# Optimization experiments

Measured on AMD Instinct MI355X. Metric: run time of the kernel, lower is better.

Reference implementation:

```python
import jax, jax.numpy as jnp
import numpy as np
from jax import lax

N_SIN = 3

def _bn(x, g, b, m, v, eps):
    sh = [1] * x.ndim; sh[1] = -1
    r = lambda t: t.reshape(sh)
    return (x - r(m)) / jnp.sqrt(r(v) + eps) * r(g) + r(b)

def _conv2d(x, w, b, padding):
    y = lax.conv_general_dilated(x, w, (1, 1), padding,
                                 dimension_numbers=('NCHW', 'OIHW', 'NCHW'))
    return y + b[None, :, None, None]

def _causal_conv1d(x, w, b):
    k = w.shape[-1]
    y = lax.conv_general_dilated(x, w, (1,), [(k - 1, 0)],
                                 dimension_numbers=('NCH', 'OIH', 'NCH'))
    return y + b[None, :, None]

def _se(x, w1, w2):
    y = x.mean(axis=2)                                   # [B,C] global avg pool
    y = jax.nn.sigmoid(jax.nn.relu(y @ w1.T) @ w2.T)
    return x * y[:, :, None]

def _kan(x, W1, W2, B1, B2):
    # x: [B,din]; per-edge tiny MLP: sin/cos embed -> linear -> silu -> linear
    omega = (2.0 ** jnp.arange(N_SIN)).astype(x.dtype)   # [n_sin]
    ox = x[..., None] * omega                            # [B,din,n_sin]
    feat = jnp.concatenate([x[..., None], jnp.sin(ox), jnp.cos(ox)], axis=-1)  # [B,din,7]
    h = jnp.einsum('bif,ijhf->bijh', feat, W1) + B1[None]  # [B,din,dout,h]
    h = jax.nn.silu(h)
    out = jnp.einsum('bijh,ijh->bij', h, W2[:, :, 0, :]) + B2[None, :, :, 0]
    return out.sum(axis=1)                               # [B,dout]

def _lstm(x, w_ih, w_hh, b_ih, b_hh):
    B, T, E = x.shape
    H = w_hh.shape[1]
    def step(carry, xt):
        h, c = carry
        g = xt @ w_ih.T + h @ w_hh.T + (b_ih + b_hh)
        i, f, gg, o = jnp.split(g, 4, axis=-1)           # torch gate order i,f,g,o
        c = jax.nn.sigmoid(f) * c + jax.nn.sigmoid(i) * jnp.tanh(gg)
        h = jax.nn.sigmoid(o) * jnp.tanh(c)
        return (h, c), h
    init = (jnp.zeros((B, H), x.dtype), jnp.zeros((B, H), x.dtype))
    _, hs = lax.scan(step, init, jnp.swapaxes(x, 0, 1))
    return jnp.swapaxes(hs, 0, 1)                        # [B,T,H]

def _cluster(hidden):
    B, T, H = hidden.shape
    last = hidden[:, -1, :]
    hn = hidden / jnp.maximum(jnp.linalg.norm(hidden, axis=-1, keepdims=True), 1e-8)
    sim = jnp.einsum('bth,bsh->bts', hn, hn)
    sim = jnp.exp(-5.5 * (1.0 - sim))
    sim = sim * (1.0 - jnp.eye(T, dtype=sim.dtype))      # zero diagonal
    # 2-D prefix sums replace the O(T) python loop over block means
    S = jnp.cumsum(jnp.cumsum(sim, axis=1), axis=2)
    Sii = jnp.diagonal(S, axis1=1, axis2=2)[:, :T - 1]   # sum of [:i,:i]
    R = S[:, -1, :T - 1]                                 # sum of [:, :i]
    C = S[:, :T - 1, -1]                                 # sum of [:i, :]
    tot = S[:, -1, -1][:, None]
    i_f = jnp.arange(1, T, dtype=sim.dtype)
    dist = (Sii / i_f**2
            + (tot - R - C + Sii) / (T - i_f)**2
            - (C - Sii) / (i_f * (T - i_f))
            - (R - Sii) / (i_f * (T - i_f)))             # [B,T-1]
    cuts = jnp.argmax(dist, axis=1) + 1                  # [B]
    mask = (jnp.arange(T)[None, :] < cuts[:, None]).astype(hidden.dtype)
    corr = (hidden * mask[:, :, None]).sum(axis=1) / cuts[:, None].astype(hidden.dtype)
    return last, corr

def reference(x, we1, be1, bn_e1_g, bn_e1_b, bn_e1_m, bn_e1_v, we2, be2, bn_e2_g, bn_e2_b, bn_e2_m, bn_e2_v, w_ih, w_hh, b_ih, b_hh, mu_W1, mu_W2, mu_B1, mu_B2, std_W1, std_W2, std_B1, std_B2, muc_W1, muc_W2, muc_B1, muc_B2, stdc_W1, stdc_W2, stdc_B1, stdc_B2, fc_W1, fc_W2, fc_B1, fc_B2, wc1, bc1, bn1_g, bn1_b, bn1_m, bn1_v, se1_w1, se1_w2, wc2, bc2, bn2_g, bn2_b, bn2_m, bn2_v, se2_w1, se2_w2, wc3, bc3, bn3_g, bn3_b, bn3_m, bn3_v, eps1, eps2):
    gelu = lambda t: jax.nn.gelu(t, approximate=False)
    x = jnp.transpose(x, (0, 2, 1))                      # shuffle: [B,T,F]->[B,F,T]
    h2d = _conv2d(x[:, None], we1, be1, 'SAME')          # [B,4E,F,T]
    h2d = gelu(_bn(h2d, bn_e1_g, bn_e1_b, bn_e1_m, bn_e1_v, 1e-5))
    h2d = _conv2d(h2d, we2, be2, 'VALID')                # [B,E,1,T]
    h2d = gelu(_bn(h2d, bn_e2_g, bn_e2_b, bn_e2_m, bn_e2_v, 1e-5))
    x_src = jnp.transpose(h2d[:, :, 0, :], (0, 2, 1))    # [B,T,E]
    hseq = _lstm(x_src, w_ih, w_hh, b_ih, b_hh)          # [B,T,H]
    out, corr = _cluster(hseq)
    mu = _kan(corr, mu_W1, mu_W2, mu_B1, mu_B2)
    std = jax.nn.softplus(_kan(corr, std_W1, std_W2, std_B1, std_B2) - 5.0)
    z = mu + std * eps1
    x_z = jnp.concatenate([out, z], axis=1)              # [B,2H]
    mu_c = _kan(x_z, muc_W1, muc_W2, muc_B1, muc_B2)
    std_c = jax.nn.softplus(_kan(x_z, stdc_W1, stdc_W2, stdc_B1, stdc_B2) - 5.0)
    x1 = mu_c + std_c * eps2                             # dropout = identity (eval)
    x2 = jnp.transpose(x, (0, 2, 1))                     # [B,T,F]: channels = seq_len
    x2 = gelu(_bn(_causal_conv1d(x2, wc1, bc1), bn1_g, bn1_b, bn1_m, bn1_v, 1e-3))
    x2 = _se(x2, se1_w1, se1_w2)
    x2 = gelu(_bn(_causal_conv1d(x2, wc2, bc2), bn2_g, bn2_b, bn2_m, bn2_v, 1e-3))
    x2 = _se(x2, se2_w1, se2_w2)
    x2 = gelu(_bn(_causal_conv1d(x2, wc3, bc3), bn3_g, bn3_b, bn3_m, bn3_v, 1e-3))
    x2 = x2.mean(axis=2)                                 # [B,conv3_nf]
    x_all = jnp.concatenate([x1, x2], axis=1)            # [B, H+conv3_nf]
    return _kan(x_all, fc_W1, fc_W2, fc_B1, fc_B2)       # [B,num_classes]

def setup_inputs():
    key = jax.random.key(0)
    ks = iter(jax.random.split(key, 128))
    f32 = jnp.float32
    def n(shape, s=0.05):
        return s * jax.random.normal(next(ks), shape, f32)
    def bn_params(c):
        g = 1.0 + 0.05 * jax.random.normal(next(ks), (c,), f32)
        b = 0.05 * jax.random.normal(next(ks), (c,), f32)
        m = 0.05 * jax.random.normal(next(ks), (c,), f32)
        v = jax.random.uniform(next(ks), (c,), f32, 0.5, 1.5)
        return g, b, m, v
    def kan_params(din, dout, h=32, feat=1 + 2 * N_SIN):
        s = (2.0 / (feat + h)) ** 0.5
        return (n((din, dout, h, feat), s), n((din, dout, 1, h), s),
                jnp.zeros((din, dout, h), f32), jnp.zeros((din, dout, 1), f32))
    B, T, F_, E, H = 32, 256, 32, 64, 128
    inp = {}
    inp['x'] = jax.random.normal(next(ks), (B, T, F_), f32)
    inp['we1'] = n((4 * E, 1, 1, 8)); inp['be1'] = n((4 * E,))
    inp['bn_e1_g'], inp['bn_e1_b'], inp['bn_e1_m'], inp['bn_e1_v'] = bn_params(4 * E)
    inp['we2'] = n((E, 4 * E, F_, 1)); inp['be2'] = n((E,))
    inp['bn_e2_g'], inp['bn_e2_b'], inp['bn_e2_m'], inp['bn_e2_v'] = bn_params(E)
    inp['w_ih'] = n((4 * H, E)); inp['w_hh'] = n((4 * H, H))
    inp['b_ih'] = n((4 * H,)); inp['b_hh'] = n((4 * H,))
    for nm, (di, do) in [('mu', (H, H)), ('std', (H, H)), ('muc', (2 * H, H)), ('stdc', (2 * H, H)), ('fc', (2 * H, 10))]:
        w1, w2, b1, b2 = kan_params(di, do)
        inp[nm + '_W1'], inp[nm + '_W2'], inp[nm + '_B1'], inp[nm + '_B2'] = w1, w2, b1, b2
    inp['wc1'] = n((128, T, 8)); inp['bc1'] = n((128,))
    inp['bn1_g'], inp['bn1_b'], inp['bn1_m'], inp['bn1_v'] = bn_params(128)
    inp['se1_w1'] = n((8, 128)); inp['se1_w2'] = n((128, 8))
    inp['wc2'] = n((256, 128, 5)); inp['bc2'] = n((256,))
    inp['bn2_g'], inp['bn2_b'], inp['bn2_m'], inp['bn2_v'] = bn_params(256)
    inp['se2_w1'] = n((16, 256)); inp['se2_w2'] = n((256, 16))
    inp['wc3'] = n((128, 256, 3)); inp['bc3'] = n((128,))
    inp['bn3_g'], inp['bn3_b'], inp['bn3_m'], inp['bn3_v'] = bn_params(128)
    inp['eps1'] = jax.random.normal(next(ks), (B, H), f32)
    inp['eps2'] = jax.random.normal(next(ks), (B, H), f32)
    return inp
```

## Files before the change

### kernel.cpp

```cpp
#include <hip/hip_runtime.h>
#include <hip/hip_bf16.h>
#include <math.h>

typedef __hip_bfloat16 bf16;

#define DEV static __device__ __forceinline__

DEV float geluf(float x){ return 0.5f*x*(1.0f + erff(x*0.70710678118654752f)); }
DEV float sigmf(float x){ return 1.0f/(1.0f + __expf(-x)); }
DEV float softplusf(float x){ return (x > 15.f) ? x : log1pf(__expf(x)); }
DEV float tanhfast(float x){ float e = __expf(2.f*x); return fmaf(-2.f, 1.f/(e+1.f), 1.f); }

typedef __attribute__((ext_vector_type(8))) short v8s;
typedef __attribute__((ext_vector_type(4))) float v4f;
typedef _Float16 f16;
typedef f16 h2 __attribute__((ext_vector_type(2)));
typedef f16 f16x8 __attribute__((ext_vector_type(8)));
typedef unsigned u32x4 __attribute__((ext_vector_type(4)));

DEV float dot2f(h2 a, h2 b, float c){
#if __has_builtin(__builtin_amdgcn_fdot2)
  return __builtin_amdgcn_fdot2(a, b, c, false);
#else
  return fmaf((float)a.y, (float)b.y, fmaf((float)a.x, (float)b.x, c));
#endif
}

DEV h2 geth2(f16x8 v, int j){ h2 r; r.x = v[2*j]; r.y = v[2*j+1]; return r; }

DEV void lds_barrier(){
  asm volatile("s_waitcnt lgkmcnt(0)" ::: "memory");
  __builtin_amdgcn_s_barrier();
  __builtin_amdgcn_sched_barrier(0);
}

enum : size_t {
  OFF_W1F   = 0,
  OFF_B1F   = 2048,
  OFF_S2E   = 2304,
  OFF_B2E   = 2368,
  OFF_WIHT  = 2432,
  OFF_BIASG = 35200,
  OFF_WHHT  = 35712,
  OFF_EPI1S = 101248,
  OFF_EPI1B = 101376,
  OFF_EPI2S = 101504,
  OFF_EPI2B = 101760,
  OFF_EPI3S = 102016,
  OFF_EPI3B = 102144,
  OFF_WE2B  = 102272,
  OFF_XSRC  = 364416,
  OFF_GX    = 888704,
  OFF_HSEQ  = 5083008,
  OFF_HN    = 6131584,
  OFF_PCOL  = 7180160,
  OFF_CCOL  = 7188352,
  OFF_CUTS  = 7196544,
  OFF_LAST  = 7196576,
  OFF_CORR  = 7200672,
  OFF_FEATA = 7204768,
  OFF_MUO   = 7233440,
  OFF_STDO  = 7237536,
  OFF_XZ    = 7241632,
  OFF_FEATB = 7249824,
  OFF_MUCO  = 7307168,
  OFF_STDCO = 7311264,
  OFF_XC1   = 7315360,
  OFF_XC2   = 7446432,
  OFF_KP    = 7708576,
  OFF_B2S   = 7741344,
  OFF_X2F   = 7839648,
  OFF_XALL  = 7843744,
  OFF_FEATC = 7851936,
  WS_FLOATS = 7909280
};

__global__ __launch_bounds__(256) void prep_kernel(
    const float* we1, const float* be1,
    const float* e1g, const float* e1b, const float* e1m, const float* e1v,
    const float* we2, const float* be2, const float* e2g, const float* e2b, const float* e2m, const float* e2v,
    const float* wih, const float* whh, const float* bih, const float* bhh,
    const float* bc1, const float* c1g, const float* c1b, const float* c1m, const float* c1v,
    const float* bc2, const float* c2g, const float* c2b, const float* c2m, const float* c2v,
    const float* bc3, const float* c3g, const float* c3b, const float* c3m, const float* c3v,
    const float* muB2, const float* sdB2, const float* mcB2, const float* scB2, const float* fcB2,
    float* ws)
{
  int idx = blockIdx.x*256 + threadIdx.x;
  if(idx < 2048){
    int o = idx>>3;
    float s = e1g[o] * rsqrtf(e1v[o] + 1e-5f);
    ws[OFF_W1F + idx] = we1[idx] * s;
  } else if(idx < 2304){
    int o = idx - 2048;
    float s = e1g[o] * rsqrtf(e1v[o] + 1e-5f);
    ws[OFF_B1F + o] = s*(be1[o] - e1m[o]) + e1b[o];
  } else if(idx < 2368){
    int e = idx - 2304;
    float s = e2g[e] * rsqrtf(e2v[e] + 1e-5f);
    ws[OFF_S2E + e] = s;
    ws[OFF_B2E + e] = s*(be2[e] - e2m[e]) + e2b[e];
  } else if(idx < 35136){
    int q = idx - 2368; int e = q>>9, g = q&511;
    ws[OFF_WIHT + q] = wih[g*64 + e];
  } else if(idx < 35648){
    int g = idx - 35136;
    ws[OFF_BIASG + g] = bih[g] + bhh[g];
  } else if(idx < 101184){
    int q = idx - 35648;
    if(q < 32768){
      int k2 = q>>9, g = q&511;
      h2 v;
      v.x = (f16)whh[g*128 + 2*k2];
      v.y = (f16)whh[g*128 + 2*k2 + 1];
      ((h2*)(ws + OFF_WHHT))[g*64 + k2] = v;
    }
  } else if(idx < 101312){
    int o = idx - 101184;
    float s = c1g[o] * rsqrtf(c1v[o] + 1e-3f);
    ws[OFF_EPI1S + o] = s;
    ws[OFF_EPI1B + o] = s*(bc1[o] - c1m[o]) + c1b[o];
  } else if(idx < 101568){
    int o = idx - 101312;
    float s = c2g[o] * rsqrtf(c2v[o] + 1e-3f);
    ws[OFF_EPI2S + o] = s;
    ws[OFF_EPI2B + o] = s*(bc2[o] - c2m[o]) + c2b[o];
  } else if(idx < 101696){
    int o = idx - 101568;
    float s = c3g[o] * rsqrtf(c3v[o] + 1e-3f);
    ws[OFF_EPI3S + o] = s;
    ws[OFF_EPI3B + o] = s*(bc3[o] - c3m[o]) + c3b[o];
  } else if(idx < 625984){
    int q = idx - 101696;
    int o = q >> 11, rem = q & 2047;
    int e = rem >> 5, f = rem & 31;
    bf16* Wr = (bf16*)(ws + OFF_WE2B);
    Wr[q] = __float2bfloat16(we2[(size_t)e*8192 + o*32 + f]);
  } else if(idx < 626112){
    int j = idx - 625984; float s = 0.f;
    for(int i=0;i<128;i++) s += muB2[i*128+j];
    ws[OFF_B2S + j] = s;
  } else if(idx < 626240){
    int j = idx - 626112; float s = 0.f;
    for(int i=0;i<128;i++) s += sdB2[i*128+j];
    ws[OFF_B2S + 128 + j] = s;
  } else if(idx < 626368){
    int j = idx - 626240; float s = 0.f;
    for(int i=0;i<256;i++) s += mcB2[i*128+j];
    ws[OFF_B2S + 256 + j] = s;
  } else if(idx < 626496){
    int j = idx - 626368; float s = 0.f;
    for(int i=0;i<256;i++) s += scB2[i*128+j];
    ws[OFF_B2S + 384 + j] = s;
  } else if(idx < 626506){
    int j = idx - 626496; float s = 0.f;
    for(int i=0;i<256;i++) s += fcB2[i*10+j];
    ws[OFF_B2S + 512 + j] = s;
  }
}

__global__ __launch_bounds__(256,1) void encoder_kernel(
    const float* __restrict__ x, const float* __restrict__ w1f, const float* __restrict__ b1f,
    const float* __restrict__ s2e, const float* __restrict__ b2e,
    const bf16* __restrict__ Wr, float* __restrict__ x_src)
{
  __shared__ float xs[39*32];
  __shared__ float w1s[2048];
  __shared__ float b1s[256];
  __shared__ __align__(16) unsigned short At[2][32*136];
  __shared__ __align__(16) unsigned short Bt[2][4*2560];

  int blk = blockIdx.x; int b = blk>>3; int t0 = (blk&7)*32;
  int tid = threadIdx.x;

  for(int i=tid;i<2048;i+=256) w1s[i] = w1f[i];
  b1s[tid] = b1f[tid];
  for(int i=tid;i<39*32;i+=256){
    int r=i>>5, f=i&31; int t=t0-3+r;
    xs[i] = (t>=0 && t<256) ? x[(b*256+t)*32+f] : 0.f;
  }
  __syncthreads();

  int f = tid & 31, tq = tid >> 5;
  int lane = tid & 63, w = tid >> 6;
  int wm = w & 1, wn = w >> 1;
  int m0 = wm*16, n0 = wn*32;
  int l15 = lane & 15, quad = lane >> 4;

  const v8s* Wv = (const v8s*)Wr;

  auto stage = [&](int cc, int buf){
    v8s bw[4];
    #pragma unroll
    for(int i=0;i<4;i++) bw[i] = Wv[cc*1024 + i*256 + tid];
    unsigned short aval[16];
    #pragma unroll
    for(int ol=0;ol<4;ol++){
      int o = cc*4 + ol;
      float wv[8];
      #pragma unroll
      for(int j=0;j<8;j++) wv[j] = w1s[o*8+j];
      float bb = b1s[o];
      #pragma unroll
      for(int i=0;i<4;i++){
        int tl = tq*4 + i;
        float c = bb;
        #pragma unroll
        for(int j=0;j<8;j++) c = fmaf(wv[j], xs[(tl+j)*32+f], c);
        aval[ol*4+i] = ((__hip_bfloat16_raw)__float2bfloat16(geluf(c))).x;
      }
    }
    #pragma unroll
    for(int ol=0;ol<4;ol++){
      #pragma unroll
      for(int i=0;i<4;i++)
        At[buf][(tq*4+i)*136 + ol*32 + f] = aval[ol*4+i];
    }
    #pragma unroll
    for(int i=0;i<4;i++){
      int j = i*256 + tid;
      int ol = j>>8, e = (j&255)>>2, f8 = j&3;
      *(v8s*)&Bt[buf][ol*2560 + e*40 + f8*8] = bw[i];
    }
  };

  stage(0, 0);
  __syncthreads();

  v4f acc0 = {0.f,0.f,0.f,0.f}, acc1 = {0.f,0.f,0.f,0.f};

  for(int c=0;c<64;c++){
    int p = c & 1, q = p ^ 1;
    if(c < 63) stage(c+1, q);
    #pragma unroll
    for(int ol=0;ol<4;ol++){
      v8s av = *(const v8s*)&At[p][(m0+l15)*136 + ol*32 + quad*8];
      v8s b0 = *(const v8s*)&Bt[p][ol*2560 + (n0+l15)*40 + quad*8];
      v8s b1 = *(const v8s*)&Bt[p][ol*2560 + (n0+16+l15)*40 + quad*8];
      acc0 = __builtin_amdgcn_mfma_f32_16x16x32_bf16(av, b0, acc0, 0, 0, 0);
      acc1 = __builtin_amdgcn_mfma_f32_16x16x32_bf16(av, b1, acc1, 0, 0, 0);
    }
    __syncthreads();
  }

  #pragma unroll
  for(int r=0;r<4;r++){
    int t = t0 + m0 + quad*4 + r;
    int e0 = n0 + l15;
    float v0 = geluf(s2e[e0]*acc0[r] + b2e[e0]);
    x_src[((size_t)(b*256+t))*64 + e0] = v0;
    int e1 = e0 + 16;
    float v1 = geluf(s2e[e1]*acc1[r] + b2e[e1]);
    x_src[((size_t)(b*256+t))*64 + e1] = v1;
  }
}

__global__ __launch_bounds__(256) void gates_kernel(
    const float* x_src, const float* wihT, const float* biasg, float* gx)
{
  __shared__ float xsh[32*64];
  int blk = blockIdx.x; int b = blk>>3, t0 = (blk&7)*32;
  int tid = threadIdx.x;
  for(int i=tid;i<2048;i+=256) xsh[i] = x_src[((size_t)b*256+t0)*64 + i];
  __syncthreads();
  int g0 = tid, g1 = tid + 256;
  float acc0[32], acc1[32];
  #pragma unroll
  for(int tt=0;tt<32;tt++){ acc0[tt]=0.f; acc1[tt]=0.f; }
  for(int e=0;e<64;e++){
    float w0 = wihT[e*512+g0], w1 = wihT[e*512+g1];
    #pragma unroll
    for(int tt=0;tt<32;tt++){
      float xv = xsh[tt*64+e];
      acc0[tt] = fmaf(xv, w0, acc0[tt]);
      acc1[tt] = fmaf(xv, w1, acc1[tt]);
    }
  }
  float bg0 = biasg[g0], bg1 = biasg[g1];
  #pragma unroll
  for(int tt=0;tt<32;tt++){
    gx[((size_t)b*256+t0+tt)*512 + g0] = acc0[tt] + bg0;
    gx[((size_t)b*256+t0+tt)*512 + g1] = acc1[tt] + bg1;
  }
}

#define LSTM_STEP(GI, GF, GG, GO, PR, PW, T)                                 \
  {                                                                          \
    const f16x8* hp = (const f16x8*)&hsh[PR][half*64];                       \
    f16x8 hvv[8];                                                            \
    _Pragma("unroll")                                                        \
    for(int q=0;q<8;q++) hvv[q] = hp[q];                                     \
    float si=0.f, sf=0.f, sg=0.f, so=0.f;                                    \
    _Pragma("unroll")                                                        \
    for(int q=0;q<8;q++){                                                    \
      f16x8 Wi = __builtin_bit_cast(f16x8, wi[q]);                           \
      f16x8 Wf = __builtin_bit_cast(f16x8, wf[q]);                           \
      f16x8 Wg = __builtin_bit_cast(f16x8, wg[q]);                           \
      f16x8 Wo = __builtin_bit_cast(f16x8, wo[q]);                           \
      f16x8 hq = hvv[q];                                                     \
      _Pragma("unroll")                                                      \
      for(int j=0;j<4;j++){                                                  \
        h2 hj = geth2(hq, j);                                                \
        si = dot2f(hj, geth2(Wi,j), si);                                     \
        sf = dot2f(hj, geth2(Wf,j), sf);                                     \
        sg = dot2f(hj, geth2(Wg,j), sg);                                     \
        so = dot2f(hj, geth2(Wo,j), so);                                     \
      }                                                                      \
    }                                                                        \
    si += __shfl_xor(si, 32, 64);                                            \
    sf += __shfl_xor(sf, 32, 64);                                            \
    sg += __shfl_xor(sg, 32, 64);                                            \
    so += __shfl_xor(so, 32, 64);                                            \
    float iv = sigmf(si + (GI));                                             \
    float fv = sigmf(sf + (GF));                                             \
    float gv = tanhfast(sg + (GG));                                          \
    float ov = sigmf(so + (GO));                                             \
    c = fmaf(fv, c, iv*gv);                                                  \
    float h = ov*tanhfast(c);                                                \
    if(half == 0){                                                           \
      hsh[PW][n] = (f16)h;                                                   \
      hseq[((size_t)b*256+(T))*128 + n] = h;                                 \
    }                                                                        \
    lds_barrier();                                                           \
  }

__global__ __launch_bounds__(256)
__attribute__((amdgpu_waves_per_eu(1,1)))
void lstm_conv_kernel(
    const float* __restrict__ gates_x, const float* __restrict__ whh16f, float* __restrict__ hseq,
    const float* __restrict__ x,
    const float* __restrict__ wc1, const float* __restrict__ wc2, const float* __restrict__ wc3,
    const float* __restrict__ epi1s, const float* __restrict__ epi1b,
    const float* __restrict__ epi2s, const float* __restrict__ epi2b,
    const float* __restrict__ epi3s, const float* __restrict__ epi3b,
    const float* __restrict__ se1w1, const float* __restrict__ se1w2,
    const float* __restrict__ se2w1, const float* __restrict__ se2w2,
    float* __restrict__ x2f)
{
  __shared__ __align__(16) f16 hsh[2][128];
  __shared__ float bufA[8192];
  __shared__ float bufB[4096];
  __shared__ float msh[256];
  __shared__ float ysh[16];

  int tid = threadIdx.x;
  if(blockIdx.x < 32){
    int b = blockIdx.x;
    int wave = tid >> 6, lane = tid & 63;
    int half = lane >> 5;
    int n = wave*32 + (lane & 31);

    const u32x4* Wp = (const u32x4*)whh16f;
    u32x4 wi[8], wf[8], wg[8], wo[8];
    #pragma unroll
    for(int q=0;q<8;q++){
      wi[q] = Wp[(size_t)(n      )*16 + half*8 + q];
      wf[q] = Wp[(size_t)(n + 128)*16 + half*8 + q];
      wg[q] = Wp[(size_t)(n + 256)*16 + half*8 + q];
      wo[q] = Wp[(size_t)(n + 384)*16 + half*8 + q];
    }
    asm volatile("" :
      "+v"(wi[0]), "+v"(wi[1]), "+v"(wi[2]), "+v"(wi[3]),
      "+v"(wi[4]), "+v"(wi[5]), "+v"(wi[6]), "+v"(wi[7]),
      "+v"(wf[0]), "+v"(wf[1]), "+v"(wf[2]), "+v"(wf[3]),
      "+v"(wf[4]), "+v"(wf[5]), "+v"(wf[6]), "+v"(wf[7]));
    asm volatile("" :
      "+v"(wg[0]), "+v"(wg[1]), "+v"(wg[2]), "+v"(wg[3]),
      "+v"(wg[4]), "+v"(wg[5]), "+v"(wg[6]), "+v"(wg[7]),
      "+v"(wo[0]), "+v"(wo[1]), "+v"(wo[2]), "+v"(wo[3]),
      "+v"(wo[4]), "+v"(wo[5]), "+v"(wo[6]), "+v"(wo[7]));

    if(tid < 128) hsh[0][tid] = (f16)0.f;
    float c = 0.f;
    const float* gx = gates_x + (size_t)b*256*512;
    float i0v = gx[n], f0v = gx[128+n], g0v = gx[256+n], o0v = gx[384+n];
    float i1v = gx[512+n], f1v = gx[512+128+n], g1v = gx[512+256+n], o1v = gx[512+384+n];
    __syncthreads();
    for(int t=0; t<256; t+=2){
      float i2v=0.f,f2v=0.f,g2v=0.f,o2v=0.f,i3v=0.f,f3v=0.f,g3v=0.f,o3v=0.f;
      if(t+2 < 256){
        const float* gp = gx + (size_t)(t+2)*512;
        i2v = gp[n]; f2v = gp[128+n]; g2v = gp[256+n]; o2v = gp[384+n];
      }
      LSTM_STEP(i0v, f0v, g0v, o0v, 0, 1, t);
      if(t+3 < 256){
        const float* gp = gx + (size_t)(t+3)*512;
        i3v = gp[n]; f3v = gp[128+n]; g3v = gp[256+n]; o3v = gp[384+n];
      }
      LSTM_STEP(i1v, f1v, g1v, o1v, 1, 0, t+1);
      i0v=i2v; f0v=f2v; g0v=g2v; o0v=o2v;
      i1v=i3v; f1v=f3v; g1v=g3v; o1v=o3v;
    }
  } else {
    int cb = blockIdx.x - 32;
    for(int i=tid; i<8192; i+=256) bufA[i] = x[(size_t)cb*8192 + i];
    __syncthreads();

    {
      int o = tid >> 1, lh = tid & 1, l0 = lh*16;
      float acc[16];
      #pragma unroll
      for(int j=0;j<16;j++) acc[j]=0.f;
      const float* wrow = wc1 + (size_t)o*2048;
      for(int c=0;c<256;c++){
        float wv[8];
        #pragma unroll
        for(int k=0;k<8;k++) wv[k] = wrow[c*8+k];
        float xr[23];
        #pragma unroll
        for(int i=0;i<23;i++){
          int li = l0 - 7 + i;
          xr[i] = (li>=0) ? bufA[c*32+li] : 0.f;
        }
        #pragma unroll
        for(int j=0;j<16;j++){
          #pragma unroll
          for(int k=0;k<8;k++) acc[j] = fmaf(xr[j+k], wv[k], acc[j]);
        }
      }
      float s = epi1s[o], bb = epi1b[o];
      float g[16]; float m = 0.f;
      #pragma unroll
      for(int j=0;j<16;j++){ g[j] = geluf(s*acc[j]+bb); m += g[j]; }
      m += __shfl_xor(m, 1, 64);
      if(lh==0) msh[o] = m*(1.f/32.f);
      __syncthreads();
      if(tid < 8){
        float t2=0.f;
        for(int k=0;k<128;k++) t2 = fmaf(msh[k], se1w1[tid*128+k], t2);
        ysh[tid] = fmaxf(t2, 0.f);
      }
      __syncthreads();
      float t2=0.f;
      #pragma unroll
      for(int k=0;k<8;k++) t2 = fmaf(ysh[k], se1w2[o*8+k], t2);
      float sc = sigmf(t2);
      #pragma unroll
      for(int j=0;j<16;j++) bufB[o*32 + l0 + j] = g[j]*sc;
      __syncthreads();
    }

    {
      int o = tid;
      float acc[32];
      #pragma unroll
      for(int j=0;j<32;j++) acc[j]=0.f;
      const float* wrow = wc2 + (size_t)o*640;
      for(int c=0;c<128;c++){
        float wv[5];
        #pragma unroll
        for(int k=0;k<5;k++) wv[k] = wrow[c*5+k];
        float xr[36];
        #pragma unroll
        for(int i=0;i<36;i++){
          int li = i - 4;
          xr[i] = (li>=0) ? bufB[c*32+li] : 0.f;
        }
        #pragma unroll
        for(int j=0;j<32;j++){
          #pragma unroll
          for(int k=0;k<5;k++) acc[j] = fmaf(xr[j+k], wv[k], acc[j]);
        }
      }
      float s = epi2s[o], bb = epi2b[o];
      float m = 0.f;
      #pragma unroll
      for(int j=0;j<32;j++){ acc[j] = geluf(s*acc[j]+bb); m += acc[j]; }
      msh[o] = m*(1.f/32.f);
      __syncthreads();
      if(tid < 16){
        float t2=0.f;
        for(int k=0;k<256;k++) t2 = fmaf(msh[k], se2w1[tid*256+k], t2);
        ysh[tid] = fmaxf(t2, 0.f);
      }
      __syncthreads();
      float t2=0.f;
      #pragma unroll
      for(int k=0;k<16;k++) t2 = fmaf(ysh[k], se2w2[o*16+k], t2);
      float sc = sigmf(t2);
      #pragma unroll
      for(int j=0;j<32;j++) bufA[o*32 + j] = acc[j]*sc;
      __syncthreads();
    }

    {
      int o = tid >> 1, lh = tid & 1, l0 = lh*16;
      float acc[16];
      #pragma unroll
      for(int j=0;j<16;j++) acc[j]=0.f;
      const float* wrow = wc3 + (size_t)o*768;
      for(int c=0;c<256;c++){
        float wv[3];
        #pragma unroll
        for(int k=0;k<3;k++) wv[k] = wrow[c*3+k];
        float xr[18];
        #pragma unroll
        for(int i=0;i<18;i++){
          int li = l0 - 2 + i;
          xr[i] = (li>=0) ? bufA[c*32+li] : 0.f;
        }
        #pragma unroll
        for(int j=0;j<16;j++){
          #pragma unroll
          for(int k=0;k<3;k++) acc[j] = fmaf(xr[j+k], wv[k], acc[j]);
        }
      }
      float s = epi3s[o], bb = epi3b[o];
      float m = 0.f;
      #pragma unroll
      for(int j=0;j<16;j++) m += geluf(s*acc[j]+bb);
      m += __shfl_xor(m, 1, 64);
      if(lh==0) x2f[cb*128 + o] = m*(1.f/32.f);
    }
  }
}

__global__ __launch_bounds__(64) void hn_kernel(const float* hseq, float* hn)
{
  size_t row = blockIdx.x; int lane = threadIdx.x;
  const float* hp = hseq + row*128;
  float v0 = hp[lane], v1 = hp[lane+64];
  float ss = v0*v0 + v1*v1;
  #pragma unroll
  for(int m=1;m<64;m<<=1) ss += __shfl_xor(ss, m, 64);
  float r = 1.f / fmaxf(sqrtf(ss), 1e-8f);
  hn[row*128 + lane]      = v0*r;
  hn[row*128 + 64 + lane] = v1*r;
}

__global__ __launch_bounds__(256) void pc_kernel(const float* hn, float* pcol, float* ccol)
{
  int blk = blockIdx.x; int b = blk>>3, chunk = blk&7;
  int tid = threadIdx.x; int il = tid & 31, ts = tid >> 5;
  int i = chunk*32 + il;
  const float4* hb = (const float4*)(hn + (size_t)b*32768);
  float4 hi[32];
  #pragma unroll
  for(int r=0;r<32;r++) hi[r] = hb[(size_t)i*32 + r];
  float ps=0.f, cs=0.f;
  for(int t=ts*32; t<ts*32+32; t++){
    float dx=0.f, dy=0.f, dz=0.f, dw=0.f;
    #pragma unroll
    for(int r=0;r<32;r++){
      float4 hv = hb[(size_t)t*32 + r];
      dx = fmaf(hi[r].x, hv.x, dx);
      dy = fmaf(hi[r].y, hv.y, dy);
      dz = fmaf(hi[r].z, hv.z, dz);
      dw = fmaf(hi[r].w, hv.w, dw);
    }
    float dot = (dx+dy)+(dz+dw);
    float sim = (t==i) ? 0.f : expf(-5.5f*(1.0f - dot));
    cs += sim;
    if(t < i) ps += sim;
  }
  __shared__ float red[16][32];
  red[ts][il] = ps; red[8+ts][il] = cs;
  __syncthreads();
  if(tid < 32){
    float s=0.f;
    for(int r=0;r<8;r++) s += red[r][tid];
    pcol[b*256 + chunk*32 + tid] = s;
  } else if(tid < 64){
    int c2 = tid - 32; float s=0.f;
    for(int r=0;r<8;r++) s += red[8+r][c2];
    ccol[b*256 + chunk*32 + c2] = s;
  }
}

__global__ __launch_bounds__(256) void cutcorr_kernel(
    const float* pcol, const float* ccol, const float* hseq,
    float* last, float* corr, int* cuts)
{
  int b = blockIdx.x, tid = threadIdx.x;
  __shared__ float D[256], RC[256], dist[256];
  __shared__ int cutsh;
  if(tid == 0){
    float d=0.f, r=0.f;
    for(int i=0;i<256;i++){
      d += 2.f*pcol[b*256+i]; D[i]=d;
      r += ccol[b*256+i];     RC[i]=r;
    }
  }
  __syncthreads();
  float tot = RC[255];
  if(tid < 255){
    float Dv = D[tid], Rv = RC[tid];
    float i_f = (float)(tid+1), j_f = 256.f - i_f;
    dist[tid] = Dv/(i_f*i_f) + (tot - 2.f*Rv + Dv)/(j_f*j_f) - 2.f*(Rv - Dv)/(i_f*j_f);
  }
  __syncthreads();
  if(tid == 0){
    float best = dist[0]; int bi = 0;
    for(int i=1;i<255;i++) if(dist[i] > best){ best = dist[i]; bi = i; }
    cutsh = bi + 1; cuts[b] = cutsh;
  }
  __syncthreads();
  int cut = cutsh;
  int k = tid & 127, half = tid >> 7;
  float s = 0.f;
  for(int t=half; t<cut; t+=2) s += hseq[((size_t)b*256+t)*128 + k];
  __shared__ float partial[2][128];
  partial[half][k] = s;
  __syncthreads();
  if(tid < 128){
    corr[b*128+tid] = (partial[0][tid] + partial[1][tid]) / (float)cut;
    last[b*128+tid] = hseq[((size_t)b*256+255)*128 + tid];
  }
}

__global__ __launch_bounds__(256) void feat_kernel(const float* xin, float* feat, int n)
{
  int idx = blockIdx.x*256 + threadIdx.x;
  if(idx >= n) return;
  float xv = xin[idx];
  float* fp = feat + (size_t)idx*7;
  fp[0]=xv;
  fp[1]=sinf(xv); fp[2]=sinf(2.f*xv); fp[3]=sinf(4.f*xv);
  fp[4]=cosf(xv); fp[5]=cosf(2.f*xv); fp[6]=cosf(4.f*xv);
}

__global__ __launch_bounds__(256) void kanp2_kernel(
    const float* __restrict__ feat,
    const float* __restrict__ W1a, const float* __restrict__ B1a, const float* __restrict__ W2a,
    const float* __restrict__ W1b, const float* __restrict__ B1b, const float* __restrict__ W2b,
    int din, int dout, float* __restrict__ partial, int pstride)
{
  __shared__ float feat_s[32*225];
  __shared__ float red[8][32];
  int z = blockIdx.z;
  const float* W1 = z ? W1b : W1a;
  const float* B1 = z ? B1b : B1a;
  const float* W2 = z ? W2b : W2a;
  partial += (size_t)z * pstride;
  int j = blockIdx.x, ic = blockIdx.y;
  int i0 = ic*32;
  int tid = threadIdx.x;
  int b = tid & 31, hg = tid >> 5;
  for(int q=tid; q<1792; q+=256){
    int br = q/56, qq = q - br*56;
    float4 v = *(const float4*)(feat + ((size_t)br*din + i0)*7 + qq*4);
    float* d = &feat_s[br*225 + qq*4];
    d[0]=v.x; d[1]=v.y; d[2]=v.z; d[3]=v.w;
  }
  __syncthreads();
  float acc = 0.f;
  const float* fb = &feat_s[b*225];
  for(int ii=0; ii<32; ii++){
    int i = i0 + ii;
    size_t hbase = ((size_t)i*dout + j)*32 + hg*4;
    const float4* w1p = (const float4*)(W1 + ((size_t)i*dout + j)*224 + hg*28);
    float w1a[28];
    #pragma unroll
    for(int q=0;q<7;q++) *(float4*)&w1a[q*4] = w1p[q];
    float4 b1v = *(const float4*)(B1 + hbase);
    float4 w2v = *(const float4*)(W2 + hbase);
    float f[7];
    #pragma unroll
    for(int q=0;q<7;q++) f[q] = fb[ii*7+q];
    float b1a[4] = {b1v.x, b1v.y, b1v.z, b1v.w};
    float w2a[4] = {w2v.x, w2v.y, w2v.z, w2v.w};
    #pragma unroll
    for(int hh=0;hh<4;hh++){
      float hv = b1a[hh];
      #pragma unroll
      for(int q=0;q<7;q++) hv = fmaf(f[q], w1a[hh*7+q], hv);
      float sv = hv / (1.f + __expf(-hv));
      acc = fmaf(sv, w2a[hh], acc);
    }
  }
  red[hg][b] = acc;
  __syncthreads();
  if(tid < 32){
    float s = 0.f;
    #pragma unroll
    for(int q=0;q<8;q++) s += red[q][tid];
    partial[((size_t)ic*32 + tid)*dout + j] = s;
  }
}

__global__ __launch_bounds__(256) void kanp_kernel(
    const float* __restrict__ feat, const float* __restrict__ W1,
    const float* __restrict__ B1, const float* __restrict__ W2,
    int din, int dout, float* __restrict__ partial)
{
  __shared__ float feat_s[32*225];
  __shared__ float red[8][32];
  int j = blockIdx.x, ic = blockIdx.y;
  int i0 = ic*32;
  int tid = threadIdx.x;
  int b = tid & 31, hg = tid >> 5;
  for(int q=tid; q<1792; q+=256){
    int br = q/56, qq = q - br*56;
    float4 v = *(const float4*)(feat + ((size_t)br*din + i0)*7 + qq*4);
    float* d = &feat_s[br*225 + qq*4];
    d[0]=v.x; d[1]=v.y; d[2]=v.z; d[3]=v.w;
  }
  __syncthreads();
  float acc = 0.f;
  const float* fb = &feat_s[b*225];
  for(int ii=0; ii<32; ii++){
    int i = i0 + ii;
    size_t hbase = ((size_t)i*dout + j)*32 + hg*4;
    const float4* w1p = (const float4*)(W1 + ((size_t)i*dout + j)*224 + hg*28);
    float w1a[28];
    #pragma unroll
    for(int q=0;q<7;q++) *(float4*)&w1a[q*4] = w1p[q];
    float4 b1v = *(const float4*)(B1 + hbase);
    float4 w2v = *(const float4*)(W2 + hbase);
    float f[7];
    #pragma unroll
    for(int q=0;q<7;q++) f[q] = fb[ii*7+q];
    float b1a[4] = {b1v.x, b1v.y, b1v.z, b1v.w};
    float w2a[4] = {w2v.x, w2v.y, w2v.z, w2v.w};
    #pragma unroll
    for(int hh=0;hh<4;hh++){
      float hv = b1a[hh];
      #pragma unroll
      for(int q=0;q<7;q++) hv = fmaf(f[q], w1a[hh*7+q], hv);
      float sv = hv / (1.f + __expf(-hv));
      acc = fmaf(sv, w2a[hh], acc);
    }
  }
  red[hg][b] = acc;
  __syncthreads();
  if(tid < 32){
    float s = 0.f;
    #pragma unroll
    for(int q=0;q<8;q++) s += red[q][tid];
    partial[((size_t)ic*32 + tid)*dout + j] = s;
  }
}

__global__ __launch_bounds__(256) void kanr_kernel(
    const float* __restrict__ partial, const float* __restrict__ b2s,
    int NI, int dout, float* __restrict__ outp)
{
  int idx = blockIdx.x*256 + threadIdx.x;
  if(idx >= 32*dout) return;
  int b = idx / dout, j = idx - b*dout;
  float s = b2s[j];
  for(int ic=0; ic<NI; ic++) s += partial[((size_t)ic*32 + b)*dout + j];
  outp[idx] = s;
}

__global__ __launch_bounds__(256) void kanrz_kernel(
    const float* __restrict__ kp, const float* __restrict__ b2s,
    const float* __restrict__ eps1, const float* __restrict__ last, float* __restrict__ xz)
{
  int idx = blockIdx.x*256 + threadIdx.x;
  if(idx >= 4096) return;
  int b = idx >> 7, j = idx & 127;
  float mu = b2s[j], sd = b2s[128+j];
  #pragma unroll
  for(int ic=0; ic<4; ic++){
    mu += kp[((size_t)ic*32 + b)*128 + j];
    sd += kp[16384 + ((size_t)ic*32 + b)*128 + j];
  }
  float z = mu + softplusf(sd - 5.f)*eps1[idx];
  xz[b*256 + j]       = last[idx];
  xz[b*256 + 128 + j] = z;
}

__global__ __launch_bounds__(256) void kanrx_kernel(
    const float* __restrict__ kp, const float* __restrict__ b2s,
    const float* __restrict__ eps2, const float* __restrict__ x2f, float* __restrict__ xa)
{
  int idx = blockIdx.x*256 + threadIdx.x;
  if(idx >= 4096) return;
  int b = idx >> 7, j = idx & 127;
  float mu = b2s[256+j], sd = b2s[384+j];
  #pragma unroll
  for(int ic=0; ic<8; ic++){
    mu += kp[((size_t)ic*32 + b)*128 + j];
    sd += kp[32768 + ((size_t)ic*32 + b)*128 + j];
  }
  xa[b*256 + j]       = mu + softplusf(sd - 5.f)*eps2[idx];
  xa[b*256 + 128 + j] = x2f[idx];
}

extern "C" void kernel_launch(void* const* d_in, const int* in_sizes, int n_in,
                              void* d_out, int out_size, void* d_ws, size_t ws_size,
                              hipStream_t stream)
{
  const float* x    = (const float*)d_in[0];
  const float* we1  = (const float*)d_in[1];
  const float* be1  = (const float*)d_in[2];
  const float* e1g  = (const float*)d_in[3];
  const float* e1b  = (const float*)d_in[4];
  const float* e1m  = (const float*)d_in[5];
  const float* e1v  = (const float*)d_in[6];
  const float* we2  = (const float*)d_in[7];
  const float* be2  = (const float*)d_in[8];
  const float* e2g  = (const float*)d_in[9];
  const float* e2b  = (const float*)d_in[10];
  const float* e2m  = (const float*)d_in[11];
  const float* e2v  = (const float*)d_in[12];
  const float* wih  = (const float*)d_in[13];
  const float* whh  = (const float*)d_in[14];
  const float* bih  = (const float*)d_in[15];
  const float* bhh  = (const float*)d_in[16];
  const float* muW1 = (const float*)d_in[17];
  const float* muW2 = (const float*)d_in[18];
  const float* muB1 = (const float*)d_in[19];
  const float* muB2 = (const float*)d_in[20];
  const float* sdW1 = (const float*)d_in[21];
  const float* sdW2 = (const float*)d_in[22];
  const float* sdB1 = (const float*)d_in[23];
  const float* sdB2 = (const float*)d_in[24];
  const float* mcW1 = (const float*)d_in[25];
  const float* mcW2 = (const float*)d_in[26];
  const float* mcB1 = (const float*)d_in[27];
  const float* mcB2 = (const float*)d_in[28];
  const float* scW1 = (const float*)d_in[29];
  const float* scW2 = (const float*)d_in[30];
  const float* scB1 = (const float*)d_in[31];
  const float* scB2 = (const float*)d_in[32];
  const float* fcW1 = (const float*)d_in[33];
  const float* fcW2 = (const float*)d_in[34];
  const float* fcB1 = (const float*)d_in[35];
  const float* fcB2 = (const float*)d_in[36];
  const float* wc1  = (const float*)d_in[37];
  const float* bc1  = (const float*)d_in[38];
  const float* c1g  = (const float*)d_in[39];
  const float* c1b  = (const float*)d_in[40];
  const float* c1m  = (const float*)d_in[41];
  const float* c1v  = (const float*)d_in[42];
  const float* se1w1= (const float*)d_in[43];
  const float* se1w2= (const float*)d_in[44];
  const float* wc2  = (const float*)d_in[45];
  const float* bc2  = (const float*)d_in[46];
  const float* c2g  = (const float*)d_in[47];
  const float* c2b  = (const float*)d_in[48];
  const float* c2m  = (const float*)d_in[49];
  const float* c2v  = (const float*)d_in[50];
  const float* se2w1= (const float*)d_in[51];
  const float* se2w2= (const float*)d_in[52];
  const float* wc3  = (const float*)d_in[53];
  const float* bc3  = (const float*)d_in[54];
  const float* c3g  = (const float*)d_in[55];
  const float* c3b  = (const float*)d_in[56];
  const float* c3m  = (const float*)d_in[57];
  const float* c3v  = (const float*)d_in[58];
  const float* eps1 = (const float*)d_in[59];
  const float* eps2 = (const float*)d_in[60];

  float* ws = (float*)d_ws;
  float* kp   = ws + OFF_KP;
  float* kp2  = ws + OFF_GX;
  float* b2s  = ws + OFF_B2S;

  prep_kernel<<<2448, 256, 0, stream>>>(we1, be1, e1g,e1b,e1m,e1v,
      we2, be2,e2g,e2b,e2m,e2v, wih,whh,bih,bhh,
      bc1,c1g,c1b,c1m,c1v, bc2,c2g,c2b,c2m,c2v, bc3,c3g,c3b,c3m,c3v,
      muB2, sdB2, mcB2, scB2, fcB2, ws);

  encoder_kernel<<<256, 256, 0, stream>>>(x, ws+OFF_W1F, ws+OFF_B1F,
      ws+OFF_S2E, ws+OFF_B2E, (const bf16*)(ws+OFF_WE2B), ws+OFF_XSRC);

  gates_kernel<<<256, 256, 0, stream>>>(ws+OFF_XSRC, ws+OFF_WIHT, ws+OFF_BIASG, ws+OFF_GX);

  lstm_conv_kernel<<<64, 256, 0, stream>>>(ws+OFF_GX, ws+OFF_WHHT, ws+OFF_HSEQ,
      x, wc1, wc2, wc3,
      ws+OFF_EPI1S, ws+OFF_EPI1B, ws+OFF_EPI2S, ws+OFF_EPI2B, ws+OFF_EPI3S, ws+OFF_EPI3B,
      se1w1, se1w2, se2w1, se2w2, ws+OFF_X2F);

  hn_kernel<<<8192, 64, 0, stream>>>(ws+OFF_HSEQ, ws+OFF_HN);
  pc_kernel<<<256, 256, 0, stream>>>(ws+OFF_HN, ws+OFF_PCOL, ws+OFF_CCOL);
  cutcorr_kernel<<<32, 256, 0, stream>>>(ws+OFF_PCOL, ws+OFF_CCOL, ws+OFF_HSEQ,
      ws+OFF_LAST, ws+OFF_CORR, (int*)(ws+OFF_CUTS));

  feat_kernel<<<16, 256, 0, stream>>>(ws+OFF_CORR, ws+OFF_FEATA, 4096);
  kanp2_kernel<<<dim3(128,4,2), 256, 0, stream>>>(ws+OFF_FEATA,
      muW1, muB1, muW2, sdW1, sdB1, sdW2, 128, 128, kp, 16384);
  kanrz_kernel<<<16, 256, 0, stream>>>(kp, b2s, eps1, ws+OFF_LAST, ws+OFF_XZ);

  feat_kernel<<<32, 256, 0, stream>>>(ws+OFF_XZ, ws+OFF_FEATB, 8192);
  kanp2_kernel<<<dim3(128,8,2), 256, 0, stream>>>(ws+OFF_FEATB,
      mcW1, mcB1, mcW2, scW1, scB1, scW2, 256, 128, kp2, 32768);
  kanrx_kernel<<<16, 256, 0, stream>>>(kp2, b2s, eps2, ws+OFF_X2F, ws+OFF_XALL);

  feat_kernel<<<32, 256, 0, stream>>>(ws+OFF_XALL, ws+OFF_FEATC, 8192);
  kanp_kernel<<<dim3(10,8), 256, 0, stream>>>(ws+OFF_FEATC, fcW1, fcB1, fcW2, 256, 10, kp);
  kanr_kernel<<<2, 256, 0, stream>>>(kp, b2s+512, 8, 10, (float*)d_out);
}
```

Before: 875.1 us.

## Vectorize conv branch with padded weights and per-wave time-half mapping

Conv weights for the second and third conv layers are repacked in the prep kernel into padded rows of 8 and 4 floats, so the conv branch of the LSTM kernel can load them as float4. Activations are read from shared memory as float4 rows instead of scalar gathers with padding checks. Threads are remapped so each wave handles one time half for 64 output channels, which keeps lanes uniform, and the cross-half reduction now goes through shared memory rather than a shuffle. This is meant to cut scalar load and bounds-check overhead in the conv branch, which runs alongside the serial LSTM blocks, at the cost of a larger prep kernel and an extra workspace read.

```diff
diff --git a/kernel.cpp b/kernel.cpp
--- a/kernel.cpp
+++ b/kernel.cpp
@@ -59,14 +59,10 @@
   OFF_LAST  = 7196576,
   OFF_CORR  = 7200672,
   OFF_FEATA = 7204768,
-  OFF_MUO   = 7233440,
-  OFF_STDO  = 7237536,
   OFF_XZ    = 7241632,
   OFF_FEATB = 7249824,
-  OFF_MUCO  = 7307168,
-  OFF_STDCO = 7311264,
-  OFF_XC1   = 7315360,
-  OFF_XC2   = 7446432,
+  OFF_WC3P  = 7315360,
+  OFF_WC2P  = 7446432,
   OFF_KP    = 7708576,
   OFF_B2S   = 7741344,
   OFF_X2F   = 7839648,
@@ -84,6 +80,7 @@
     const float* bc2, const float* c2g, const float* c2b, const float* c2m, const float* c2v,
     const float* bc3, const float* c3g, const float* c3b, const float* c3m, const float* c3v,
     const float* muB2, const float* sdB2, const float* mcB2, const float* scB2, const float* fcB2,
+    const float* wc2, const float* wc3,
     float* ws)
 {
   int idx = blockIdx.x*256 + threadIdx.x;
@@ -156,6 +153,16 @@
     int j = idx - 626496; float s = 0.f;
     for(int i=0;i<256;i++) s += fcB2[i*10+j];
     ws[OFF_B2S + 512 + j] = s;
+  } else if(idx < 888650){
+    int q = idx - 626506;
+    int o = q >> 10, rem = q & 1023;
+    int c = rem >> 3, k = rem & 7;
+    ws[OFF_WC2P + q] = (k < 5) ? wc2[(size_t)o*640 + c*5 + k] : 0.f;
+  } else if(idx < 1019722){
+    int q = idx - 888650;
+    int o = q >> 10, rem = q & 1023;
+    int c = rem >> 2, k = rem & 3;
+    ws[OFF_WC3P + q] = (k < 3) ? wc3[(size_t)o*768 + c*3 + k] : 0.f;
   }
 }
 
@@ -329,7 +336,7 @@
 void lstm_conv_kernel(
     const float* __restrict__ gates_x, const float* __restrict__ whh16f, float* __restrict__ hseq,
     const float* __restrict__ x,
-    const float* __restrict__ wc1, const float* __restrict__ wc2, const float* __restrict__ wc3,
+    const float* __restrict__ wc1, const float* __restrict__ wc2p, const float* __restrict__ wc3p,
     const float* __restrict__ epi1s, const float* __restrict__ epi1b,
     const float* __restrict__ epi2s, const float* __restrict__ epi2b,
     const float* __restrict__ epi3s, const float* __restrict__ epi3b,
@@ -338,8 +345,8 @@
     float* __restrict__ x2f)
 {
   __shared__ __align__(16) f16 hsh[2][128];
-  __shared__ float bufA[8192];
-  __shared__ float bufB[4096];
+  __shared__ __align__(16) float bufA[8192];
+  __shared__ __align__(16) float bufB[4096];
   __shared__ float msh[256];
   __shared__ float ysh[16];
 
@@ -396,121 +403,161 @@
     for(int i=tid; i<8192; i+=256) bufA[i] = x[(size_t)cb*8192 + i];
     __syncthreads();
 
+    int wv_ = tid >> 6, ln = tid & 63;
+    int lh = wv_ >> 1;
+    int o  = ((wv_ & 1) << 6) | ln;
+
     {
-      int o = tid >> 1, lh = tid & 1, l0 = lh*16;
       float acc[16];
       #pragma unroll
       for(int j=0;j<16;j++) acc[j]=0.f;
-      const float* wrow = wc1 + (size_t)o*2048;
-      for(int c=0;c<256;c++){
-        float wv[8];
-        #pragma unroll
-        for(int k=0;k<8;k++) wv[k] = wrow[c*8+k];
-        float xr[23];
-        #pragma unroll
-        for(int i=0;i<23;i++){
-          int li = l0 - 7 + i;
-          xr[i] = (li>=0) ? bufA[c*32+li] : 0.f;
+      const float4* wp = (const float4*)(wc1 + (size_t)o*2048);
+      if(lh == 0){
+        for(int c=0;c<256;c++){
+          const float4* rp = (const float4*)&bufA[c*32];
+          float4 r0=rp[0], r1=rp[1], r2=rp[2], r3=rp[3];
+          float xr[16]={r0.x,r0.y,r0.z,r0.w,r1.x,r1.y,r1.z,r1.w,
+                        r2.x,r2.y,r2.z,r2.w,r3.x,r3.y,r3.z,r3.w};
+          float4 w0=wp[2*c], w1=wp[2*c+1];
+          float wv[8]={w0.x,w0.y,w0.z,w0.w,w1.x,w1.y,w1.z,w1.w};
+          #pragma unroll
+          for(int j=0;j<16;j++){
+            #pragma unroll
+            for(int k=0;k<8;k++){
+              int idx = j + k - 7;
+              if(idx >= 0) acc[j] = fmaf(xr[idx], wv[k], acc[j]);
+            }
+          }
         }
-        #pragma unroll
-        for(int j=0;j<16;j++){
+      } else {
+        for(int c=0;c<256;c++){
+          const float4* rp = (const float4*)&bufA[c*32];
+          float4 r2=rp[2], r3=rp[3], r4=rp[4], r5=rp[5], r6=rp[6], r7=rp[7];
+          float xr[24]={r2.x,r2.y,r2.z,r2.w,r3.x,r3.y,r3.z,r3.w,
+                        r4.x,r4.y,r4.z,r4.w,r5.x,r5.y,r5.z,r5.w,
+                        r6.x,r6.y,r6.z,r6.w,r7.x,r7.y,r7.z,r7.w};
+          float4 w0=wp[2*c], w1=wp[2*c+1];
+          float wv[8]={w0.x,w0.y,w0.z,w0.w,w1.x,w1.y,w1.z,w1.w};
           #pragma unroll
-          for(int k=0;k<8;k++) acc[j] = fmaf(xr[j+k], wv[k], acc[j]);
+          for(int j=0;j<16;j++){
+            #pragma unroll
+            for(int k=0;k<8;k++)
+              acc[j] = fmaf(xr[j+k+1], wv[k], acc[j]);
+          }
         }
       }
       float s = epi1s[o], bb = epi1b[o];
       float g[16]; float m = 0.f;
       #pragma unroll
       for(int j=0;j<16;j++){ g[j] = geluf(s*acc[j]+bb); m += g[j]; }
-      m += __shfl_xor(m, 1, 64);
-      if(lh==0) msh[o] = m*(1.f/32.f);
+      msh[lh*128 + o] = m;
       __syncthreads();
       if(tid < 8){
-        float t2=0.f;
-        for(int k=0;k<128;k++) t2 = fmaf(msh[k], se1w1[tid*128+k], t2);
+        float t2 = 0.f;
+        for(int k=0;k<128;k++) t2 = fmaf((msh[k]+msh[128+k])*(1.f/32.f), se1w1[tid*128+k], t2);
         ysh[tid] = fmaxf(t2, 0.f);
       }
       __syncthreads();
-      float t2=0.f;
+      float t2 = 0.f;
       #pragma unroll
       for(int k=0;k<8;k++) t2 = fmaf(ysh[k], se1w2[o*8+k], t2);
       float sc = sigmf(t2);
       #pragma unroll
-      for(int j=0;j<16;j++) bufB[o*32 + l0 + j] = g[j]*sc;
+      for(int j=0;j<16;j++) bufB[o*32 + lh*16 + j] = g[j]*sc;
       __syncthreads();
     }
 
     {
-      int o = tid;
+      int oc = tid;
       float acc[32];
       #pragma unroll
       for(int j=0;j<32;j++) acc[j]=0.f;
-      const float* wrow = wc2 + (size_t)o*640;
+      const float4* wp = (const float4*)(wc2p + (size_t)oc*1024);
       for(int c=0;c<128;c++){
-        float wv[5];
-        #pragma unroll
-        for(int k=0;k<5;k++) wv[k] = wrow[c*5+k];
-        float xr[36];
-        #pragma unroll
-        for(int i=0;i<36;i++){
-          int li = i - 4;
-          xr[i] = (li>=0) ? bufB[c*32+li] : 0.f;
-        }
+        const float4* rp = (const float4*)&bufB[c*32];
+        float4 r0=rp[0],r1=rp[1],r2=rp[2],r3=rp[3],r4=rp[4],r5=rp[5],r6=rp[6],r7=rp[7];
+        float xr[32]={r0.x,r0.y,r0.z,r0.w,r1.x,r1.y,r1.z,r1.w,
+                      r2.x,r2.y,r2.z,r2.w,r3.x,r3.y,r3.z,r3.w,
+                      r4.x,r4.y,r4.z,r4.w,r5.x,r5.y,r5.z,r5.w,
+                      r6.x,r6.y,r6.z,r6.w,r7.x,r7.y,r7.z,r7.w};
+        float4 w0=wp[2*c], w1=wp[2*c+1];
+        float wv[5]={w0.x,w0.y,w0.z,w0.w,w1.x};
         #pragma unroll
         for(int j=0;j<32;j++){
           #pragma unroll
-          for(int k=0;k<5;k++) acc[j] = fmaf(xr[j+k], wv[k], acc[j]);
+          for(int k=0;k<5;k++){
+            int idx = j + k - 4;
+            if(idx >= 0) acc[j] = fmaf(xr[idx], wv[k], acc[j]);
+          }
         }
       }
-      float s = epi2s[o], bb = epi2b[o];
+      float s = epi2s[oc], bb = epi2b[oc];
       float m = 0.f;
       #pragma unroll
       for(int j=0;j<32;j++){ acc[j] = geluf(s*acc[j]+bb); m += acc[j]; }
-      msh[o] = m*(1.f/32.f);
+      msh[oc] = m*(1.f/32.f);
       __syncthreads();
       if(tid < 16){
-        float t2=0.f;
+        float t2 = 0.f;
         for(int k=0;k<256;k++) t2 = fmaf(msh[k], se2w1[tid*256+k], t2);
         ysh[tid] = fmaxf(t2, 0.f);
       }
       __syncthreads();
-      float t2=0.f;
-      #pragma unroll
-      for(int k=0;k<16;k++) t2 = fmaf(ysh[k], se2w2[o*16+k], t2);
+      float t2 = 0.f;
+      #pragma unroll
+      for(int k=0;k<16;k++) t2 = fmaf(ysh[k], se2w2[oc*16+k], t2);
       float sc = sigmf(t2);
       #pragma unroll
-      for(int j=0;j<32;j++) bufA[o*32 + j] = acc[j]*sc;
+      for(int j=0;j<32;j++) bufA[oc*32 + j] = acc[j]*sc;
       __syncthreads();
     }
 
     {
-      int o = tid >> 1, lh = tid & 1, l0 = lh*16;
       float acc[16];
       #pragma unroll
       for(int j=0;j<16;j++) acc[j]=0.f;
-      const float* wrow = wc3 + (size_t)o*768;
-      for(int c=0;c<256;c++){
-        float wv[3];
-        #pragma unroll
-        for(int k=0;k<3;k++) wv[k] = wrow[c*3+k];
-        float xr[18];
-        #pragma unroll
-        for(int i=0;i<18;i++){
-          int li = l0 - 2 + i;
-          xr[i] = (li>=0) ? bufA[c*32+li] : 0.f;
+      const float4* wp = (const float4*)(wc3p + (size_t)o*1024);
+      if(lh == 0){
+        for(int c=0;c<256;c++){
+          const float4* rp = (const float4*)&bufA[c*32];
+          float4 r0=rp[0], r1=rp[1], r2=rp[2], r3=rp[3];
+          float xr[16]={r0.x,r0.y,r0.z,r0.w,r1.x,r1.y,r1.z,r1.w,
+                        r2.x,r2.y,r2.z,r2.w,r3.x,r3.y,r3.z,r3.w};
+          float4 w = wp[c];
+          float wv[3]={w.x,w.y,w.z};
+          #pragma unroll
+          for(int j=0;j<16;j++){
+            #pragma unroll
+            for(int k=0;k<3;k++){
+              int idx = j + k - 2;
+              if(idx >= 0) acc[j] = fmaf(xr[idx], wv[k], acc[j]);
+            }
+          }
         }
-        #pragma unroll
-        for(int j=0;j<16;j++){
+      } else {
+        for(int c=0;c<256;c++){
+          const float4* rp = (const float4*)&bufA[c*32];
+          float4 r3=rp[3], r4=rp[4], r5=rp[5], r6=rp[6], r7=rp[7];
+          float xr[20]={r3.x,r3.y,r3.z,r3.w,r4.x,r4.y,r4.z,r4.w,
+                        r5.x,r5.y,r5.z,r5.w,r6.x,r6.y,r6.z,r6.w,
+                        r7.x,r7.y,r7.z,r7.w};
+          float4 w = wp[c];
+          float wv[3]={w.x,w.y,w.z};
           #pragma unroll
-          for(int k=0;k<3;k++) acc[j] = fmaf(xr[j+k], wv[k], acc[j]);
+          for(int j=0;j<16;j++){
+            #pragma unroll
+            for(int k=0;k<3;k++)
+              acc[j] = fmaf(xr[j+k+2], wv[k], acc[j]);
+          }
         }
       }
       float s = epi3s[o], bb = epi3b[o];
       float m = 0.f;
       #pragma unroll
       for(int j=0;j<16;j++) m += geluf(s*acc[j]+bb);
-      m += __shfl_xor(m, 1, 64);
-      if(lh==0) x2f[cb*128 + o] = m*(1.f/32.f);
+      msh[lh*128 + o] = m;
+      __syncthreads();
+      if(tid < 128) x2f[cb*128 + tid] = (msh[tid] + msh[128+tid])*(1.f/32.f);
     }
   }
 }
@@ -849,10 +896,10 @@
   float* kp2  = ws + OFF_GX;
   float* b2s  = ws + OFF_B2S;
 
-  prep_kernel<<<2448, 256, 0, stream>>>(we1, be1, e1g,e1b,e1m,e1v,
+  prep_kernel<<<3984, 256, 0, stream>>>(we1, be1, e1g,e1b,e1m,e1v,
       we2, be2,e2g,e2b,e2m,e2v, wih,whh,bih,bhh,
       bc1,c1g,c1b,c1m,c1v, bc2,c2g,c2b,c2m,c2v, bc3,c3g,c3b,c3m,c3v,
-      muB2, sdB2, mcB2, scB2, fcB2, ws);
+      muB2, sdB2, mcB2, scB2, fcB2, wc2, wc3, ws);
 
   encoder_kernel<<<256, 256, 0, stream>>>(x, ws+OFF_W1F, ws+OFF_B1F,
       ws+OFF_S2E, ws+OFF_B2E, (const bf16*)(ws+OFF_WE2B), ws+OFF_XSRC);
@@ -860,7 +907,7 @@
   gates_kernel<<<256, 256, 0, stream>>>(ws+OFF_XSRC, ws+OFF_WIHT, ws+OFF_BIASG, ws+OFF_GX);
 
   lstm_conv_kernel<<<64, 256, 0, stream>>>(ws+OFF_GX, ws+OFF_WHHT, ws+OFF_HSEQ,
-      x, wc1, wc2, wc3,
+      x, wc1, ws+OFF_WC2P, ws+OFF_WC3P,
       ws+OFF_EPI1S, ws+OFF_EPI1B, ws+OFF_EPI2S, ws+OFF_EPI2B, ws+OFF_EPI3S, ws+OFF_EPI3B,
       se1w1, se1w2, se2w1, se2w2, ws+OFF_X2F);
 
```

Measured after the change: 866.6 us. Within noise of the previous version (-1.0%).
